# Performance work log

Hardware: AMD Instinct MI355X
Metric: run time of the kernel (lower is better)

Reference implementation:

```python
import jax, jax.numpy as jnp
import numpy as np

H = 1024      # hidden_size
MEL = 128     # mel_bins
B = 32        # batch
TENC = 512    # encoder time steps
TMEL = 400    # decoder (mel) time steps


def setup_inputs() -> dict:
    key = jax.random.key(0)
    ks = jax.random.split(key, 16)
    def w(k, shape, s=0.02):
        return jax.random.normal(k, shape, dtype=jnp.float32) * s
    return dict(
        encoder_hidden=w(ks[0], (4, B, H), 0.1),
        encoder_outputs=w(ks[1], (B, TENC, H), 0.1),
        y=w(ks[2], (B, TMEL, MEL), 1.0),
        mel_spec_lens=jax.random.randint(ks[3], (B,), 1, TMEL),
        # attention linear
        W_attn=w(ks[4], (H, H)), b_attn=jnp.zeros((H,), jnp.float32),
        # GRU layer 0 (input MEL) and layer 1 (input H); gate order r,z,n as in torch
        W_ih0=w(ks[5], (3 * H, MEL)), W_hh0=w(ks[6], (3 * H, H)),
        b_ih0=jnp.zeros((3 * H,), jnp.float32), b_hh0=jnp.zeros((3 * H,), jnp.float32),
        W_ih1=w(ks[7], (3 * H, H)), W_hh1=w(ks[8], (3 * H, H)),
        b_ih1=jnp.zeros((3 * H,), jnp.float32), b_hh1=jnp.zeros((3 * H,), jnp.float32),
        # concat2hidden, mel projection, eos gate
        Wc=w(ks[9], (H, 2 * H)), bc=jnp.zeros((H,), jnp.float32),
        Wp=w(ks[10], (MEL, H)), bp=jnp.zeros((MEL,), jnp.float32),
        Wg=w(ks[11], (1, H)), bg=jnp.zeros((1,), jnp.float32),
    )


def gru_cell(x, h, Wih, Whh, bih, bhh):
    # torch GRUCell math: gates ordered (r, z, n)
    gi = x @ Wih.T + bih          # [B, 3H]
    gh = h @ Whh.T + bhh          # [B, 3H]
    ir, iz, inn = jnp.split(gi, 3, axis=-1)
    hr, hz, hn = jnp.split(gh, 3, axis=-1)
    r = jax.nn.sigmoid(ir + hr)
    z = jax.nn.sigmoid(iz + hz)
    n = jnp.tanh(inn + r * hn)
    return (1.0 - z) * n + z * h


def reference(encoder_hidden, encoder_outputs, y, mel_spec_lens,
              W_attn, b_attn,
              W_ih0, W_hh0, b_ih0, b_hh0,
              W_ih1, W_hh1, b_ih1, b_hh1,
              Wc, bc, Wp, bp, Wg, bg):
    Bsz, Tmel, mel = y.shape
    # attention energy depends only on encoder_outputs -> hoist out of the loop (same math)
    energy = encoder_outputs @ W_attn.T + b_attn          # [B, Te, H]
    h0 = encoder_hidden[0]                                 # decoder_hidden = encoder_hidden[:num_layers]
    h1 = encoder_hidden[1]
    dec_in0 = jnp.zeros((Bsz, mel), y.dtype)               # SOS frame

    def step(carry, _):
        dec_in, h0, h1 = carry
        h0 = gru_cell(dec_in, h0, W_ih0, W_hh0, b_ih0, b_hh0)
        h1 = gru_cell(h0, h1, W_ih1, W_hh1, b_ih1, b_hh1)   # rnn_output = top-layer state [B, H]
        scores = jnp.einsum('bh,bth->bt', h1, energy)       # additive-style dot scores [B, Te]
        probs = jax.nn.softmax(scores, axis=1)
        context = jnp.einsum('bt,bth->bh', probs, encoder_outputs)  # [B, H]
        co = jnp.tanh(jnp.concatenate([h1, context], axis=-1) @ Wc.T + bc)  # [B, H]
        mel_out = co @ Wp.T + bp                            # [B, MEL]
        gate = (co @ Wg.T + bg)[:, 0]                       # [B]
        return (mel_out, h0, h1), (mel_out, gate)

    _, (mels, gates) = jax.lax.scan(step, (dec_in0, h0, h1), None, length=Tmel)
    mels = jnp.transpose(mels, (1, 0, 2))                   # [B, T, MEL]
    gates = gates.T                                          # [B, T]

    t = jnp.arange(Tmel)
    mask = t[None, :] > mel_spec_lens[:, None]               # strictly-greater, as in source
    masked_mel = jnp.where(mask[:, :, None], 0.0, mels)
    masked_gate = jnp.where(mask, 1000.0, gates)
    return masked_mel, masked_gate, mask
```

## Files before the change

### kernel.cpp

```cpp
#include <hip/hip_runtime.h>
#include <stdint.h>
#include <stddef.h>


#define TM 400

typedef unsigned short ushort_t;
typedef short  short8  __attribute__((ext_vector_type(8)));
typedef float  float4v __attribute__((ext_vector_type(4)));

#define DEVI static __device__ __forceinline__

#define SB_WF   0
#define SB_IH1  3145728
#define SB_HH0  6291456
#define SB_HH1  9437184
#define SB_AT   12582912
#define SB_WC   13631488
#define SW_TOT  15728640

__device__ __align__(16) ushort_t g_sw[SW_TOT];
__device__ __align__(16) float    g_wf[3145728];
__device__ __align__(16) ushort_t g_encb[16777216];
__device__ __align__(16) ushort_t g_energy[16777216];
__device__ __align__(16) ushort_t g_h0b[32768], g_h1b[32768];
__device__ __align__(16) float    g_h0f[32768], g_h1f[32768];
__device__ __align__(16) float    g_b0f[3072];
__device__ __align__(16) float    g_gh0[98304], g_gh1[98304];
__device__ __align__(16) float    g_ctxn[32768], g_sden[32];
__device__ __align__(16) float    g_cof[32768];
__device__ __align__(16) ushort_t g_cob[32768];

DEVI ushort_t f2b(float f) {
  union { float f; uint32_t u; } c; c.f = f;
  uint32_t u = c.u + 0x7fffu + ((c.u >> 16) & 1u);
  return (ushort_t)(u >> 16);
}
DEVI float b2f(ushort_t b) {
  union { uint32_t u; float f; } c; c.u = ((uint32_t)b) << 16; return c.f;
}
DEVI float sigm(float x) { return 1.f / (1.f + __expf(-x)); }

DEVI float4v mfma16(short8 a, short8 b, float4v c) {
  return __builtin_amdgcn_mfma_f32_16x16x32_bf16(a, b, c, 0, 0, 0);
}

DEVI float4v gemm_plain(const ushort_t* Ab, const ushort_t* Bw,
                        int ntile, int mu, int lane) {
  float4v acc = {0.f, 0.f, 0.f, 0.f};
  const ushort_t* a = Ab + (size_t)(mu * 16 + (lane & 15)) * 1024 + ((lane >> 4) << 3);
  const ushort_t* b = Bw + ((size_t)ntile * 32 * 64 + lane) * 8;
  for (int kb = 0; kb < 32; ++kb) {
    short8 av = *(const short8*)(a + kb * 32);
    acc = mfma16(av, *(const short8*)(b + (size_t)kb * 512), acc);
  }
  return acc;
}

DEVI float4v gemm_coE(const ushort_t* h1b, const float* ctxn, const float* sden,
                      const ushort_t* Bw, int ntile, int mu, int lane) {
  float4v acc = {0.f, 0.f, 0.f, 0.f};
  const int m = mu * 16 + (lane & 15), ko = (lane >> 4) << 3;
  const ushort_t* a0 = h1b + (size_t)m * 1024 + ko;
  const float* a1 = ctxn + (size_t)m * 1024 + ko;
  const float den = sden[m];
  const float inv = (den > 1e-35f) ? (1.f / den) : 0.f;
  const ushort_t* b = Bw + ((size_t)ntile * 64 * 64 + lane) * 8;
  for (int kb = 0; kb < 32; ++kb)
    acc = mfma16(*(const short8*)(a0 + kb * 32),
                 *(const short8*)(b + (size_t)kb * 512), acc);
  for (int kb = 32; kb < 64; ++kb) {
    float4v w0 = *(const float4v*)(a1 + (kb - 32) * 32);
    float4v w1 = *(const float4v*)(a1 + (kb - 32) * 32 + 4);
    short8 av;
#pragma unroll
    for (int j = 0; j < 4; ++j) {
      av[j]     = (short)f2b(w0[j] * inv);
      av[4 + j] = (short)f2b(w1[j] * inv);
    }
    acc = mfma16(av, *(const short8*)(b + (size_t)kb * 512), acc);
  }
  return acc;
}

DEVI void put_tile(float* sh, int q, int lane, float4v a) {
  const int base = q * 256 + (lane & 15);
#pragma unroll
  for (int i = 0; i < 4; ++i) sh[base + ((lane >> 4) * 4 + i) * 16] = a[i];
}

__global__ void k_wf(const float* __restrict__ Wih0, const float* __restrict__ Wp) {
  __shared__ __align__(16) float As[32][128];
  __shared__ __align__(16) float Bs[128][64];
  const int tid = threadIdx.x;
  const int nt = blockIdx.x >> 4, kt = blockIdx.x & 15;
  const int n0 = nt * 32, k0 = kt * 64;
  {
    const int r = tid >> 3, c0 = (tid & 7) * 16;
    for (int i = 0; i < 16; i += 4)
      *(float4v*)&As[r][c0 + i] = *(const float4v*)&Wih0[(size_t)(n0 + r) * 128 + c0 + i];
  }
  {
    const int r = tid >> 1, c0 = (tid & 1) * 32;
    for (int i = 0; i < 32; i += 4)
      *(float4v*)&Bs[r][c0 + i] = *(const float4v*)&Wp[(size_t)r * 1024 + k0 + c0 + i];
  }
  __syncthreads();
  const int rn = tid >> 3, kq = (tid & 7) * 8;
  float acc[8] = {0.f, 0.f, 0.f, 0.f, 0.f, 0.f, 0.f, 0.f};
  for (int m = 0; m < 128; ++m) {
    const float a = As[rn][m];
#pragma unroll
    for (int j = 0; j < 8; ++j) acc[j] += a * Bs[m][kq + j];
  }
  float* dst = g_wf + (size_t)(n0 + rn) * 1024 + k0 + kq;
#pragma unroll
  for (int j = 0; j < 8; ++j) dst[j] = acc[j];
}

__global__ void k_encb(const float* __restrict__ enc) {
  const size_t i = ((size_t)blockIdx.x * 256 + threadIdx.x) * 8;
  if (i >= 16777216) return;
  float4v a = *(const float4v*)(enc + i);
  float4v b = *(const float4v*)(enc + i + 4);
  short8 r;
#pragma unroll
  for (int j = 0; j < 4; ++j) { r[j] = (short)f2b(a[j]); r[4 + j] = (short)f2b(b[j]); }
  *(short8*)(g_encb + i) = r;
}

__global__ void k_swz(const float* __restrict__ W1, const float* __restrict__ W2,
                      const float* __restrict__ W3, const float* __restrict__ WA,
                      const float* __restrict__ WC) {
  long fid = (long)blockIdx.x * 256 + threadIdx.x;
  if (fid >= 1966080) return;
  const float* src; int N, K; long base, local;
  if      (fid < 393216)  { src = g_wf; N = 3072; K = 1024; base = SB_WF;  local = fid; }
  else if (fid < 786432)  { src = W1;   N = 3072; K = 1024; base = SB_IH1; local = fid - 393216; }
  else if (fid < 1179648) { src = W2;   N = 3072; K = 1024; base = SB_HH0; local = fid - 786432; }
  else if (fid < 1572864) { src = W3;   N = 3072; K = 1024; base = SB_HH1; local = fid - 1179648; }
  else if (fid < 1703936) { src = WA;   N = 1024; K = 1024; base = SB_AT;  local = fid - 1572864; }
  else                    { src = WC;   N = 1024; K = 2048; base = SB_WC;  local = fid - 1703936; }
  const int L = (int)(local & 63);
  long rest = local >> 6;
  const int KB = K >> 5;
  const int kb = (int)(rest % KB);
  const int nt = (int)(rest / KB);
  const int n  = nt * 16 + (L & 15);
  const int k0 = kb * 32 + ((L >> 4) << 3);
  short8 r;
#pragma unroll
  for (int i = 0; i < 8; ++i)
    r[i] = (short)f2b(src[(size_t)n * K + (k0 + i)]);
  *(short8*)(g_sw + base + local * 8) = r;
}

__global__ void k_energy(const float* __restrict__ b_attn) {
  __shared__ __align__(16) float sh[2048];
  const int tid = threadIdx.x, lane = tid & 63, wv = tid >> 6;
  const int rt = blockIdx.x;
  const ushort_t* Ab = g_encb + (size_t)rt * 32 * 1024;
  float* shw = sh + wv * 512;
  for (int i = 0; i < 16; ++i) {
    const int nt = wv * 16 + i;
    put_tile(shw, 0, lane, gemm_plain(Ab, g_sw + SB_AT, nt, 0, lane));
    put_tile(shw, 1, lane, gemm_plain(Ab, g_sw + SB_AT, nt, 1, lane));
    __syncthreads();
    const int row = lane >> 1, cf = (lane & 1) * 8;
    const int q = row >> 4, r = row & 15;
    short8 o;
#pragma unroll
    for (int j = 0; j < 8; ++j) {
      const int n = nt * 16 + cf + j;
      o[j] = (short)f2b(shw[q * 256 + r * 16 + cf + j] + b_attn[n]);
    }
    *(short8*)(g_energy + (size_t)(rt * 32 + row) * 1024 + nt * 16 + cf) = o;
    __syncthreads();
  }
}

__global__ void k_init(const float* __restrict__ ehid, const int* __restrict__ lens,
                       const float* __restrict__ Wih0, const float* __restrict__ bp,
                       const float* __restrict__ bih0,
                       float* __restrict__ out, int out_size) {
  int i = blockIdx.x * 256 + threadIdx.x;
  if (i < 32768) { float v = ehid[i]; g_h0f[i] = v; g_h0b[i] = f2b(v); }
  else if (i < 65536) {
    int j = i - 32768; float v = ehid[32768 + j];
    g_h1f[j] = v; g_h1b[j] = f2b(v);
  } else if (i < 78336) {
    int mi = i - 65536; int b = mi / 400, tt = mi % 400;
    int idx = 1651200 + mi;
    if (idx < out_size) out[idx] = (tt > lens[b]) ? 1.0f : 0.0f;
  } else if (i < 81408) {
    int n = i - 78336;
    float s = bih0[n];
    const float* wr = Wih0 + (size_t)n * 128;
    for (int m = 0; m < 128; ++m) s += bp[m] * wr[m];
    g_b0f[n] = s;
  }
}

__global__ void k_pre(const float* __restrict__ b_hh0, const float* __restrict__ b_hh1) {
  const int wg = blockIdx.x, tid = threadIdx.x;
  const int lane = tid & 63, wv = tid >> 6;
  __shared__ __align__(16) float sh[1536];
  const int qa = (wv < 2) ? wv * 2 : wv + 2;
  const int qb = (wv < 2) ? wv * 2 + 1 : -1;
  const ushort_t* Ab = (wg < 64) ? g_h0b : g_h1b;
  const ushort_t* Bw = g_sw + ((wg < 64) ? SB_HH0 : SB_HH1);
  const float* bhh = (wg < 64) ? b_hh0 : b_hh1;
  float* ghb = (wg < 64) ? g_gh0 : g_gh1;
  const int w16 = wg & 63;
  { int g = qa >> 1, mu = qa & 1;
    put_tile(sh, qa, lane, gemm_plain(Ab, Bw, g * 64 + w16, mu, lane)); }
  if (qb >= 0) { int g = qb >> 1, mu = qb & 1;
    put_tile(sh, qb, lane, gemm_plain(Ab, Bw, g * 64 + w16, mu, lane)); }
  __syncthreads();
  const int jl = tid & 15, mr = tid >> 4, jg = w16 * 16 + jl;
#pragma unroll
  for (int mu = 0; mu < 2; ++mu) {
    const int b = mu * 16 + mr;
#pragma unroll
    for (int g = 0; g < 3; ++g)
      ghb[b * 3072 + g * 1024 + jg] = sh[(g * 2 + mu) * 256 + tid] + bhh[g * 1024 + jg];
  }
}

__global__ void k_s1(int t, const float* __restrict__ b_ih0, const float* __restrict__ bp,
                     const float* __restrict__ Wp, const float* __restrict__ Wg,
                     const float* __restrict__ bg, const int* __restrict__ lens,
                     float* __restrict__ out, int out_size) {
  const int wg = blockIdx.x, tid = threadIdx.x;
  const int lane = tid & 63, wv = tid >> 6;
  __shared__ __align__(16) float sh[1536];
  if (wg < 64) {
    if (t >= TM) return;
    const int qa = (wv < 2) ? wv * 2 : wv + 2;
    const int qb = (wv < 2) ? wv * 2 + 1 : -1;
    const ushort_t* SW = g_sw + SB_WF;
    float4v acc;
    { int g = qa >> 1, mu = qa & 1;
      acc = (t > 0) ? gemm_plain(g_cob, SW, g * 64 + wg, mu, lane)
                    : float4v{0.f, 0.f, 0.f, 0.f};
      put_tile(sh, qa, lane, acc); }
    if (qb >= 0) { int g = qb >> 1, mu = qb & 1;
      acc = (t > 0) ? gemm_plain(g_cob, SW, g * 64 + wg, mu, lane)
                    : float4v{0.f, 0.f, 0.f, 0.f};
      put_tile(sh, qb, lane, acc); }
    __syncthreads();
    const int jl = tid & 15, mr = tid >> 4, jg = wg * 16 + jl;
    const float* bs = (t > 0) ? g_b0f : b_ih0;
    const float bir = bs[jg], biz = bs[1024 + jg], bin = bs[2048 + jg];
#pragma unroll
    for (int mu = 0; mu < 2; ++mu) {
      const int b = mu * 16 + mr;
      float gr = sh[mu * 256 + tid]       + bir + g_gh0[b * 3072 + jg];
      float gz = sh[(2 + mu) * 256 + tid] + biz + g_gh0[b * 3072 + 1024 + jg];
      float gn = sh[(4 + mu) * 256 + tid] + bin;
      float r = sigm(gr), z = sigm(gz);
      float nn = tanhf(gn + r * g_gh0[b * 3072 + 2048 + jg]);
      float h = (1.f - z) * nn + z * g_h0f[b * 1024 + jg];
      g_h0f[b * 1024 + jg] = h; g_h0b[b * 1024 + jg] = f2b(h);
    }
  } else if (wg < 128) {
    if (t == 0) return;
    const int idx = wg - 64, b = idx & 31, mh = idx >> 5;
    *(float4v*)&sh[tid * 4] = *(const float4v*)(g_cof + b * 1024 + tid * 4);
    __syncthreads();
    const int m = mh * 64 + (tid >> 2), q = tid & 3;
    const float* cop = sh + q * 256;
    const float* wpp = Wp + (size_t)m * 1024 + q * 256;
    float s = 0.f;
#pragma unroll 8
    for (int k = 0; k < 256; k += 4) {
      float4v cv = *(const float4v*)(cop + k);
      float4v wv4 = *(const float4v*)(wpp + k);
      s += cv[0] * wv4[0] + cv[1] * wv4[1] + cv[2] * wv4[2] + cv[3] * wv4[3];
    }
    s += __shfl_xor(s, 1, 64);
    s += __shfl_xor(s, 2, 64);
    if (q == 0) {
      const bool mk = (t - 1) > lens[b];
      const float v = mk ? 0.f : (s + bp[m]);
      const int oidx = b * 51200 + (t - 1) * 128 + m;
      if (oidx < out_size) out[oidx] = v;
    }
  } else if (wg == 128) {
    if (t == 0) return;
    const int b = tid >> 3, seg = tid & 7;
    const float* cop = g_cof + b * 1024 + seg * 128;
    const float* wgp = Wg + seg * 128;
    float s = 0.f;
#pragma unroll 8
    for (int k = 0; k < 128; k += 4) {
      float4v cv = *(const float4v*)(cop + k);
      float4v wv4 = *(const float4v*)(wgp + k);
      s += cv[0] * wv4[0] + cv[1] * wv4[1] + cv[2] * wv4[2] + cv[3] * wv4[3];
    }
    for (int o = 1; o < 8; o <<= 1) s += __shfl_xor(s, o, 64);
    if (seg == 0) {
      const bool mk = (t - 1) > lens[b];
      const float g = mk ? 1000.f : (s + bg[0]);
      const int oidx = 1638400 + b * 400 + (t - 1);
      if (oidx < out_size) out[oidx] = g;
    }
  } else {
    const int z0 = (wg - 129) * 256 + tid;
#pragma unroll
    for (int r4 = 0; r4 < 16; ++r4) g_ctxn[z0 + r4 * 2048] = 0.f;
    if (wg == 129 && tid < 32) g_sden[tid] = 0.f;
  }
}

__global__ void k_s2(const float* __restrict__ b_ih1, const float* __restrict__ b_hh0) {
  const int wg = blockIdx.x, tid = threadIdx.x;
  const int lane = tid & 63, wv = tid >> 6;
  __shared__ __align__(16) float sh[1536];
  const int qa = (wv < 2) ? wv * 2 : wv + 2;
  const int qb = (wv < 2) ? wv * 2 + 1 : -1;
  const bool lo = (wg < 64);
  const int w16 = wg & 63;
  const ushort_t* SW = g_sw + (lo ? SB_IH1 : SB_HH0);
  { int g = qa >> 1, mu = qa & 1;
    put_tile(sh, qa, lane, gemm_plain(g_h0b, SW, g * 64 + w16, mu, lane)); }
  if (qb >= 0) { int g = qb >> 1, mu = qb & 1;
    put_tile(sh, qb, lane, gemm_plain(g_h0b, SW, g * 64 + w16, mu, lane)); }
  __syncthreads();
  const int jl = tid & 15, mr = tid >> 4, jg = w16 * 16 + jl;
  if (lo) {
    const float bir = b_ih1[jg], biz = b_ih1[1024 + jg], bin = b_ih1[2048 + jg];
#pragma unroll
    for (int mu = 0; mu < 2; ++mu) {
      const int b = mu * 16 + mr;
      float gr = sh[mu * 256 + tid]       + bir + g_gh1[b * 3072 + jg];
      float gz = sh[(2 + mu) * 256 + tid] + biz + g_gh1[b * 3072 + 1024 + jg];
      float gn = sh[(4 + mu) * 256 + tid] + bin;
      float r = sigm(gr), z = sigm(gz);
      float nn = tanhf(gn + r * g_gh1[b * 3072 + 2048 + jg]);
      float h = (1.f - z) * nn + z * g_h1f[b * 1024 + jg];
      g_h1f[b * 1024 + jg] = h; g_h1b[b * 1024 + jg] = f2b(h);
    }
  } else {
#pragma unroll
    for (int mu = 0; mu < 2; ++mu) {
      const int b = mu * 16 + mr;
#pragma unroll
      for (int g = 0; g < 3; ++g)
        g_gh0[b * 3072 + g * 1024 + jg] = sh[(g * 2 + mu) * 256 + tid] + b_hh0[g * 1024 + jg];
    }
  }
}

__global__ void k_s3() {
  __shared__ __align__(16) float sh[4160];
  const int wg = blockIdx.x, tid = threadIdx.x;
  const int lane = tid & 63, wv = tid >> 6;
  const int b = wg >> 3, slot = wg & 7;
  const float* hp = g_h1f + b * 1024;
  float u0[8], u1[8];
  {
    float4v a0 = *(const float4v*)(hp + lane * 8);
    float4v a1 = *(const float4v*)(hp + lane * 8 + 4);
    float4v b0 = *(const float4v*)(hp + 512 + lane * 8);
    float4v b1 = *(const float4v*)(hp + 512 + lane * 8 + 4);
#pragma unroll
    for (int j = 0; j < 4; ++j) {
      u0[j] = a0[j]; u0[4 + j] = a1[j];
      u1[j] = b0[j]; u1[4 + j] = b1[j];
    }
  }
  float cx0[8] = {0.f, 0.f, 0.f, 0.f, 0.f, 0.f, 0.f, 0.f};
  float cx1[8] = {0.f, 0.f, 0.f, 0.f, 0.f, 0.f, 0.f, 0.f};
  float sw = 0.f;
  const size_t base = ((size_t)(b * 512 + slot * 64 + wv * 16)) * 1024 + lane * 8;
  for (int it = 0; it < 16; ++it) {
    const size_t off = base + (size_t)it * 1024;
    short8 g0 = *(const short8*)(g_energy + off);
    short8 g1 = *(const short8*)(g_energy + off + 512);
    short8 e0 = *(const short8*)(g_encb + off);
    short8 e1 = *(const short8*)(g_encb + off + 512);
    float ef0[8], ef1[8];
    float s = 0.f;
#pragma unroll
    for (int j = 0; j < 8; ++j) {
      ef0[j] = b2f((ushort_t)e0[j]);
      ef1[j] = b2f((ushort_t)e1[j]);
      s += u0[j] * b2f((ushort_t)g0[j]) + u1[j] * b2f((ushort_t)g1[j]);
    }
    for (int o = 1; o < 64; o <<= 1) s += __shfl_xor(s, o, 64);
    const float sc = fminf(fmaxf(s, -70.f), 70.f);
    const float p = __expf(sc);
    sw += p;
#pragma unroll
    for (int j = 0; j < 8; ++j) { cx0[j] += p * ef0[j]; cx1[j] += p * ef1[j]; }
  }
#pragma unroll
  for (int j = 0; j < 8; ++j) {
    sh[wv * 1024 + lane * 8 + j]       = cx0[j];
    sh[wv * 1024 + 512 + lane * 8 + j] = cx1[j];
  }
  if (lane == 0) sh[4096 + wv] = sw;
  __syncthreads();
  float4v t4 = {0.f, 0.f, 0.f, 0.f};
#pragma unroll
  for (int v = 0; v < 4; ++v) t4 += *(const float4v*)&sh[v * 1024 + tid * 4];
  float* dst = g_ctxn + b * 1024 + tid * 4;
#pragma unroll
  for (int c = 0; c < 4; ++c) unsafeAtomicAdd(dst + c, t4[c]);
  if (tid == 0)
    unsafeAtomicAdd(&g_sden[b], sh[4096] + sh[4097] + sh[4098] + sh[4099]);
}

__global__ void k_s4(const float* __restrict__ bc, const float* __restrict__ b_hh1) {
  const int wg = blockIdx.x, tid = threadIdx.x;
  const int lane = tid & 63, wv = tid >> 6;
  __shared__ __align__(16) float sh[1536];
  if (wg < 64) {
    if (wv < 2)
      put_tile(sh, wv, lane, gemm_coE(g_h1b, g_ctxn, g_sden, g_sw + SB_WC, wg, wv, lane));
    __syncthreads();
    const int jl = tid & 15, mr = tid >> 4;
    const float bcv = bc[wg * 16 + jl];
#pragma unroll
    for (int mu = 0; mu < 2; ++mu) {
      const int b = mu * 16 + mr;
      const float v = tanhf(sh[mu * 256 + tid] + bcv);
      g_cof[b * 1024 + wg * 16 + jl] = v;
      g_cob[b * 1024 + wg * 16 + jl] = f2b(v);
    }
  } else {
    const int w16 = wg - 64;
    const int qa = (wv < 2) ? wv * 2 : wv + 2;
    const int qb = (wv < 2) ? wv * 2 + 1 : -1;
    { int g = qa >> 1, mu = qa & 1;
      put_tile(sh, qa, lane, gemm_plain(g_h1b, g_sw + SB_HH1, g * 64 + w16, mu, lane)); }
    if (qb >= 0) { int g = qb >> 1, mu = qb & 1;
      put_tile(sh, qb, lane, gemm_plain(g_h1b, g_sw + SB_HH1, g * 64 + w16, mu, lane)); }
    __syncthreads();
    const int jl = tid & 15, mr = tid >> 4, jg = w16 * 16 + jl;
#pragma unroll
    for (int mu = 0; mu < 2; ++mu) {
      const int b = mu * 16 + mr;
#pragma unroll
      for (int g = 0; g < 3; ++g)
        g_gh1[b * 3072 + g * 1024 + jg] = sh[(g * 2 + mu) * 256 + tid] + b_hh1[g * 1024 + jg];
    }
  }
}

extern "C" void kernel_launch(void* const* d_in, const int* in_sizes, int n_in,
                              void* d_out, int out_size, void* d_ws, size_t ws_size,
                              hipStream_t stream) {
  const float* ehid  = (const float*)d_in[0];
  const float* enc   = (const float*)d_in[1];
  const int*   lens  = (const int*)d_in[3];
  const float* W_attn= (const float*)d_in[4];
  const float* b_attn= (const float*)d_in[5];
  const float* W_ih0 = (const float*)d_in[6];
  const float* W_hh0 = (const float*)d_in[7];
  const float* b_ih0 = (const float*)d_in[8];
  const float* b_hh0 = (const float*)d_in[9];
  const float* W_ih1 = (const float*)d_in[10];
  const float* W_hh1 = (const float*)d_in[11];
  const float* b_ih1 = (const float*)d_in[12];
  const float* b_hh1 = (const float*)d_in[13];
  const float* Wc    = (const float*)d_in[14];
  const float* bc    = (const float*)d_in[15];
  const float* Wp    = (const float*)d_in[16];
  const float* bp    = (const float*)d_in[17];
  const float* Wg    = (const float*)d_in[18];
  const float* bg    = (const float*)d_in[19];
  float* out = (float*)d_out;

  k_wf    <<<1536, 256, 0, stream>>>(W_ih0, Wp);
  k_encb  <<<8192, 256, 0, stream>>>(enc);
  k_swz   <<<7680, 256, 0, stream>>>(W_ih1, W_hh0, W_hh1, W_attn, Wc);
  k_energy<<<512,  256, 0, stream>>>(b_attn);
  k_init  <<<318,  256, 0, stream>>>(ehid, lens, W_ih0, bp, b_ih0, out, out_size);
  k_pre   <<<128,  256, 0, stream>>>(b_hh0, b_hh1);
  for (int t = 0; t < TM; ++t) {
    k_s1<<<137, 256, 0, stream>>>(t, b_ih0, bp, Wp, Wg, bg, lens, out, out_size);
    k_s2<<<128, 256, 0, stream>>>(b_ih1, b_hh0);
    k_s3<<<256, 256, 0, stream>>>();
    k_s4<<<128, 256, 0, stream>>>(bc, b_hh1);
  }
  k_s1<<<137, 256, 0, stream>>>(TM, b_ih0, bp, Wp, Wg, bg, lens, out, out_size);
}
```

Baseline: 21.23 ms.

## Quantize attention energy/encoder to fp8, fuse attention and concat stages, MFMA mel projection

Energy and encoder outputs are stored as fp8 e4m3 bytes and decoded through a shared-memory lookup table, halving the bytes streamed in the per-step attention kernel. The attention and concat/GRU-hh1 kernels are merged into one launch, with an atomic counter spin-wait so the concat blocks start only after all attention blocks finish. The mel projection is moved to bf16 MFMA using a pre-swizzled Wp. Risks include fp8 precision loss, and a possible deadlock or timeout fallback if the waiting blocks get scheduled before the producer blocks.

Result: slower. 24.69 ms (+16.3%).

```diff
diff --git a/kernel.cpp b/kernel.cpp
--- a/kernel.cpp
+++ b/kernel.cpp
@@ -6,8 +6,10 @@
 #define TM 400
 
 typedef unsigned short ushort_t;
-typedef short  short8  __attribute__((ext_vector_type(8)));
-typedef float  float4v __attribute__((ext_vector_type(4)));
+typedef unsigned long long u64_t;
+typedef short    short8  __attribute__((ext_vector_type(8)));
+typedef float    float4v __attribute__((ext_vector_type(4)));
+typedef unsigned uint2v  __attribute__((ext_vector_type(2)));
 
 #define DEVI static __device__ __forceinline__
 
@@ -17,12 +19,14 @@
 #define SB_HH1  9437184
 #define SB_AT   12582912
 #define SB_WC   13631488
-#define SW_TOT  15728640
+#define SB_WP   15728640
+#define SW_TOT  15859712
 
 __device__ __align__(16) ushort_t g_sw[SW_TOT];
 __device__ __align__(16) float    g_wf[3145728];
 __device__ __align__(16) ushort_t g_encb[16777216];
-__device__ __align__(16) ushort_t g_energy[16777216];
+__device__ __align__(16) unsigned char g_en8[16777216];
+__device__ __align__(16) unsigned char g_ec8[16777216];
 __device__ __align__(16) ushort_t g_h0b[32768], g_h1b[32768];
 __device__ __align__(16) float    g_h0f[32768], g_h1f[32768];
 __device__ __align__(16) float    g_b0f[3072];
@@ -30,19 +34,46 @@
 __device__ __align__(16) float    g_ctxn[32768], g_sden[32];
 __device__ __align__(16) float    g_cof[32768];
 __device__ __align__(16) ushort_t g_cob[32768];
+__device__ __align__(64) unsigned g_done[16];
 
 DEVI ushort_t f2b(float f) {
   union { float f; uint32_t u; } c; c.f = f;
   uint32_t u = c.u + 0x7fffu + ((c.u >> 16) & 1u);
   return (ushort_t)(u >> 16);
 }
-DEVI float b2f(ushort_t b) {
-  union { uint32_t u; float f; } c; c.u = ((uint32_t)b) << 16; return c.f;
-}
 DEVI float sigm(float x) { return 1.f / (1.f + __expf(-x)); }
+
+DEVI unsigned char f2e4m3(float f) {
+  union { float f; uint32_t u; } c; c.f = f;
+  const unsigned s = (c.u >> 24) & 0x80u;
+  const float a = fabsf(f);
+  if (a >= 448.f) return (unsigned char)(s | 0x7Eu);
+  if (a < 0.015625f) {
+    int m = (int)(a * 512.f + 0.5f);
+    if (m >= 8) return (unsigned char)(s | 0x08u);
+    return (unsigned char)(s | (unsigned)m);
+  }
+  int e32 = (int)((c.u >> 23) & 0xffu);
+  uint32_t m3 = (c.u >> 20) & 7u;
+  const uint32_t rem = c.u & 0xfffffu;
+  if (rem > 0x80000u || (rem == 0x80000u && (m3 & 1u))) {
+    if (++m3 == 8u) { m3 = 0u; ++e32; }
+  }
+  const int e8 = e32 - 120;
+  if (e8 >= 16) return (unsigned char)(s | 0x7Eu);
+  return (unsigned char)(s | ((unsigned)e8 << 3) | m3);
+}
 
 DEVI float4v mfma16(short8 a, short8 b, float4v c) {
   return __builtin_amdgcn_mfma_f32_16x16x32_bf16(a, b, c, 0, 0, 0);
+}
+
+DEVI u64_t ld_sc8(const void* p) {
+  return __hip_atomic_load((const u64_t*)p, __ATOMIC_RELAXED,
+                           __HIP_MEMORY_SCOPE_SYSTEM);
+}
+DEVI float ld_scf(const float* p) {
+  return __hip_atomic_load(p, __ATOMIC_RELAXED, __HIP_MEMORY_SCOPE_SYSTEM);
 }
 
 DEVI float4v gemm_plain(const ushort_t* Ab, const ushort_t* Bw,
@@ -57,28 +88,36 @@
   return acc;
 }
 
-DEVI float4v gemm_coE(const ushort_t* h1b, const float* ctxn, const float* sden,
-                      const ushort_t* Bw, int ntile, int mu, int lane) {
+DEVI float4v gemm_scE2(const ushort_t* h1b, const float* ctxn, const float* sden,
+                       const ushort_t* Bw, int ntile, int mu, int lane) {
   float4v acc = {0.f, 0.f, 0.f, 0.f};
   const int m = mu * 16 + (lane & 15), ko = (lane >> 4) << 3;
   const ushort_t* a0 = h1b + (size_t)m * 1024 + ko;
   const float* a1 = ctxn + (size_t)m * 1024 + ko;
-  const float den = sden[m];
+  const float den = ld_scf(&sden[m]);
   const float inv = (den > 1e-35f) ? (1.f / den) : 0.f;
   const ushort_t* b = Bw + ((size_t)ntile * 64 * 64 + lane) * 8;
   for (int kb = 0; kb < 32; ++kb)
     acc = mfma16(*(const short8*)(a0 + kb * 32),
                  *(const short8*)(b + (size_t)kb * 512), acc);
-  for (int kb = 32; kb < 64; ++kb) {
-    float4v w0 = *(const float4v*)(a1 + (kb - 32) * 32);
-    float4v w1 = *(const float4v*)(a1 + (kb - 32) * 32 + 4);
-    short8 av;
-#pragma unroll
-    for (int j = 0; j < 4; ++j) {
-      av[j]     = (short)f2b(w0[j] * inv);
-      av[4 + j] = (short)f2b(w1[j] * inv);
-    }
-    acc = mfma16(av, *(const short8*)(b + (size_t)kb * 512), acc);
+  for (int c = 0; c < 4; ++c) {
+    u64_t t[32];
+#pragma unroll
+    for (int j = 0; j < 8; ++j)
+#pragma unroll
+      for (int q = 0; q < 4; ++q)
+        t[j * 4 + q] = ld_sc8(a1 + (c * 8 + j) * 32 + q * 2);
+#pragma unroll
+    for (int j = 0; j < 8; ++j) {
+      short8 av;
+#pragma unroll
+      for (int q = 0; q < 4; ++q) {
+        union { u64_t u; float f[2]; } w; w.u = t[j * 4 + q];
+        av[q * 2]     = (short)f2b(w.f[0] * inv);
+        av[q * 2 + 1] = (short)f2b(w.f[1] * inv);
+      }
+      acc = mfma16(av, *(const short8*)(b + (size_t)(32 + c * 8 + j) * 512), acc);
+    }
   }
   return acc;
 }
@@ -129,18 +168,34 @@
   *(short8*)(g_encb + i) = r;
 }
 
+__global__ void k_q8(const float* __restrict__ enc) {
+  const size_t i = ((size_t)blockIdx.x * 256 + threadIdx.x) * 8;
+  if (i >= 16777216) return;
+  float4v a = *(const float4v*)(enc + i);
+  float4v b = *(const float4v*)(enc + i + 4);
+  unsigned lo = 0, hi = 0;
+#pragma unroll
+  for (int j = 0; j < 4; ++j) {
+    lo |= (unsigned)f2e4m3(a[j]) << (8 * j);
+    hi |= (unsigned)f2e4m3(b[j]) << (8 * j);
+  }
+  uint2v o; o[0] = lo; o[1] = hi;
+  *(uint2v*)(g_ec8 + i) = o;
+}
+
 __global__ void k_swz(const float* __restrict__ W1, const float* __restrict__ W2,
                       const float* __restrict__ W3, const float* __restrict__ WA,
-                      const float* __restrict__ WC) {
+                      const float* __restrict__ WC, const float* __restrict__ Wp) {
   long fid = (long)blockIdx.x * 256 + threadIdx.x;
-  if (fid >= 1966080) return;
+  if (fid >= 1982464) return;
   const float* src; int N, K; long base, local;
   if      (fid < 393216)  { src = g_wf; N = 3072; K = 1024; base = SB_WF;  local = fid; }
   else if (fid < 786432)  { src = W1;   N = 3072; K = 1024; base = SB_IH1; local = fid - 393216; }
   else if (fid < 1179648) { src = W2;   N = 3072; K = 1024; base = SB_HH0; local = fid - 786432; }
   else if (fid < 1572864) { src = W3;   N = 3072; K = 1024; base = SB_HH1; local = fid - 1179648; }
   else if (fid < 1703936) { src = WA;   N = 1024; K = 1024; base = SB_AT;  local = fid - 1572864; }
-  else                    { src = WC;   N = 1024; K = 2048; base = SB_WC;  local = fid - 1703936; }
+  else if (fid < 1966080) { src = WC;   N = 1024; K = 2048; base = SB_WC;  local = fid - 1703936; }
+  else                    { src = Wp;   N = 128;  K = 1024; base = SB_WP;  local = fid - 1966080; }
   const int L = (int)(local & 63);
   long rest = local >> 6;
   const int KB = K >> 5;
@@ -168,13 +223,14 @@
     __syncthreads();
     const int row = lane >> 1, cf = (lane & 1) * 8;
     const int q = row >> 4, r = row & 15;
-    short8 o;
-#pragma unroll
-    for (int j = 0; j < 8; ++j) {
-      const int n = nt * 16 + cf + j;
-      o[j] = (short)f2b(shw[q * 256 + r * 16 + cf + j] + b_attn[n]);
-    }
-    *(short8*)(g_energy + (size_t)(rt * 32 + row) * 1024 + nt * 16 + cf) = o;
+    unsigned lo = 0, hi = 0;
+#pragma unroll
+    for (int j = 0; j < 4; ++j) {
+      lo |= (unsigned)f2e4m3(shw[q * 256 + r * 16 + cf + j] + b_attn[nt * 16 + cf + j]) << (8 * j);
+      hi |= (unsigned)f2e4m3(shw[q * 256 + r * 16 + cf + 4 + j] + b_attn[nt * 16 + cf + 4 + j]) << (8 * j);
+    }
+    uint2v o; o[0] = lo; o[1] = hi;
+    *(uint2v*)(g_en8 + (size_t)(rt * 32 + row) * 1024 + nt * 16 + cf) = o;
     __syncthreads();
   }
 }
@@ -184,6 +240,7 @@
                        const float* __restrict__ bih0,
                        float* __restrict__ out, int out_size) {
   int i = blockIdx.x * 256 + threadIdx.x;
+  if (i == 0) g_done[0] = 0u;
   if (i < 32768) { float v = ehid[i]; g_h0f[i] = v; g_h0b[i] = f2b(v); }
   else if (i < 65536) {
     int j = i - 32768; float v = ehid[32768 + j];
@@ -228,8 +285,8 @@
 }
 
 __global__ void k_s1(int t, const float* __restrict__ b_ih0, const float* __restrict__ bp,
-                     const float* __restrict__ Wp, const float* __restrict__ Wg,
-                     const float* __restrict__ bg, const int* __restrict__ lens,
+                     const float* __restrict__ Wg, const float* __restrict__ bg,
+                     const int* __restrict__ lens,
                      float* __restrict__ out, int out_size) {
   const int wg = blockIdx.x, tid = threadIdx.x;
   const int lane = tid & 63, wv = tid >> 6;
@@ -263,30 +320,24 @@
       float h = (1.f - z) * nn + z * g_h0f[b * 1024 + jg];
       g_h0f[b * 1024 + jg] = h; g_h0b[b * 1024 + jg] = f2b(h);
     }
-  } else if (wg < 128) {
+  } else if (wg < 72) {
     if (t == 0) return;
-    const int idx = wg - 64, b = idx & 31, mh = idx >> 5;
-    *(float4v*)&sh[tid * 4] = *(const float4v*)(g_cof + b * 1024 + tid * 4);
-    __syncthreads();
-    const int m = mh * 64 + (tid >> 2), q = tid & 3;
-    const float* cop = sh + q * 256;
-    const float* wpp = Wp + (size_t)m * 1024 + q * 256;
-    float s = 0.f;
-#pragma unroll 8
-    for (int k = 0; k < 256; k += 4) {
-      float4v cv = *(const float4v*)(cop + k);
-      float4v wv4 = *(const float4v*)(wpp + k);
-      s += cv[0] * wv4[0] + cv[1] * wv4[1] + cv[2] * wv4[2] + cv[3] * wv4[3];
-    }
-    s += __shfl_xor(s, 1, 64);
-    s += __shfl_xor(s, 2, 64);
-    if (q == 0) {
+    const int nt = wg - 64;
+    if (wv < 2)
+      put_tile(sh, wv, lane, gemm_plain(g_cob, g_sw + SB_WP, nt, wv, lane));
+    __syncthreads();
+    const int jl = tid & 15, mr = tid >> 4;
+    const int m = nt * 16 + jl;
+    const float bpv = bp[m];
+#pragma unroll
+    for (int mu = 0; mu < 2; ++mu) {
+      const int b = mu * 16 + mr;
       const bool mk = (t - 1) > lens[b];
-      const float v = mk ? 0.f : (s + bp[m]);
+      const float v = mk ? 0.f : (sh[mu * 256 + tid] + bpv);
       const int oidx = b * 51200 + (t - 1) * 128 + m;
       if (oidx < out_size) out[oidx] = v;
     }
-  } else if (wg == 128) {
+  } else if (wg == 72) {
     if (t == 0) return;
     const int b = tid >> 3, seg = tid & 7;
     const float* cop = g_cof + b * 1024 + seg * 128;
@@ -306,10 +357,13 @@
       if (oidx < out_size) out[oidx] = g;
     }
   } else {
-    const int z0 = (wg - 129) * 256 + tid;
+    const int z0 = (wg - 73) * 256 + tid;
 #pragma unroll
     for (int r4 = 0; r4 < 16; ++r4) g_ctxn[z0 + r4 * 2048] = 0.f;
-    if (wg == 129 && tid < 32) g_sden[tid] = 0.f;
+    if (wg == 73 && tid < 32) g_sden[tid] = 0.f;
+    if (wg == 73 && tid == 0)
+      __hip_atomic_store(&g_done[0], 0u, __ATOMIC_RELAXED,
+                         __HIP_MEMORY_SCOPE_AGENT);
   }
 }
 
@@ -352,85 +406,109 @@
   }
 }
 
-__global__ void k_s3() {
+__global__ void k_s34(const float* __restrict__ bc, const float* __restrict__ b_hh1) {
   __shared__ __align__(16) float sh[4160];
+  __shared__ __align__(16) float tabf[256];
   const int wg = blockIdx.x, tid = threadIdx.x;
   const int lane = tid & 63, wv = tid >> 6;
-  const int b = wg >> 3, slot = wg & 7;
-  const float* hp = g_h1f + b * 1024;
-  float u0[8], u1[8];
-  {
-    float4v a0 = *(const float4v*)(hp + lane * 8);
-    float4v a1 = *(const float4v*)(hp + lane * 8 + 4);
-    float4v b0 = *(const float4v*)(hp + 512 + lane * 8);
-    float4v b1 = *(const float4v*)(hp + 512 + lane * 8 + 4);
-#pragma unroll
-    for (int j = 0; j < 4; ++j) {
-      u0[j] = a0[j]; u0[4 + j] = a1[j];
-      u1[j] = b0[j]; u1[4 + j] = b1[j];
-    }
-  }
-  float cx0[8] = {0.f, 0.f, 0.f, 0.f, 0.f, 0.f, 0.f, 0.f};
-  float cx1[8] = {0.f, 0.f, 0.f, 0.f, 0.f, 0.f, 0.f, 0.f};
-  float sw = 0.f;
-  const size_t base = ((size_t)(b * 512 + slot * 64 + wv * 16)) * 1024 + lane * 8;
-  for (int it = 0; it < 16; ++it) {
-    const size_t off = base + (size_t)it * 1024;
-    short8 g0 = *(const short8*)(g_energy + off);
-    short8 g1 = *(const short8*)(g_energy + off + 512);
-    short8 e0 = *(const short8*)(g_encb + off);
-    short8 e1 = *(const short8*)(g_encb + off + 512);
-    float ef0[8], ef1[8];
-    float s = 0.f;
+  if (wg < 256) {
+    {
+      const unsigned v = (unsigned)tid;
+      const unsigned e = (v >> 3) & 0xFu, m = v & 7u;
+      union { unsigned u; float f; } c;
+      if (e == 0u) c.f = (float)m * 0.001953125f;
+      else c.u = ((e + 120u) << 23) | (m << 20);
+      c.u |= (v & 0x80u) << 24;
+      tabf[v] = c.f;
+    }
+    const int b = wg >> 3, slot = wg & 7;
+    const float* hp = g_h1f + b * 1024;
+    float u0[8], u1[8];
+    {
+      float4v a0 = *(const float4v*)(hp + lane * 8);
+      float4v a1 = *(const float4v*)(hp + lane * 8 + 4);
+      float4v b0 = *(const float4v*)(hp + 512 + lane * 8);
+      float4v b1 = *(const float4v*)(hp + 512 + lane * 8 + 4);
+#pragma unroll
+      for (int j = 0; j < 4; ++j) {
+        u0[j] = a0[j]; u0[4 + j] = a1[j];
+        u1[j] = b0[j]; u1[4 + j] = b1[j];
+      }
+    }
+    __syncthreads();
+    float cx0[8] = {0.f, 0.f, 0.f, 0.f, 0.f, 0.f, 0.f, 0.f};
+    float cx1[8] = {0.f, 0.f, 0.f, 0.f, 0.f, 0.f, 0.f, 0.f};
+    float sw = 0.f;
+    const size_t base = ((size_t)(b * 512 + slot * 64 + wv * 16)) * 1024 + lane * 8;
+    for (int it = 0; it < 16; ++it) {
+      const size_t off = base + (size_t)it * 1024;
+      uint2v gE0 = *(const uint2v*)(g_en8 + off);
+      uint2v gE1 = *(const uint2v*)(g_en8 + off + 512);
+      uint2v eE0 = *(const uint2v*)(g_ec8 + off);
+      uint2v eE1 = *(const uint2v*)(g_ec8 + off + 512);
+      float ef0[8], ef1[8];
+      float s = 0.f;
+#pragma unroll
+      for (int w = 0; w < 2; ++w)
+#pragma unroll
+        for (int j = 0; j < 4; ++j) {
+          const int k = w * 4 + j;
+          s += u0[k] * tabf[(gE0[w] >> (8 * j)) & 0xffu];
+          s += u1[k] * tabf[(gE1[w] >> (8 * j)) & 0xffu];
+          ef0[k] = tabf[(eE0[w] >> (8 * j)) & 0xffu];
+          ef1[k] = tabf[(eE1[w] >> (8 * j)) & 0xffu];
+        }
+      for (int o = 1; o < 64; o <<= 1) s += __shfl_xor(s, o, 64);
+      const float sc = fminf(fmaxf(s, -70.f), 70.f);
+      const float p = __expf(sc);
+      sw += p;
+#pragma unroll
+      for (int j = 0; j < 8; ++j) { cx0[j] += p * ef0[j]; cx1[j] += p * ef1[j]; }
+    }
 #pragma unroll
     for (int j = 0; j < 8; ++j) {
-      ef0[j] = b2f((ushort_t)e0[j]);
-      ef1[j] = b2f((ushort_t)e1[j]);
-      s += u0[j] * b2f((ushort_t)g0[j]) + u1[j] * b2f((ushort_t)g1[j]);
-    }
-    for (int o = 1; o < 64; o <<= 1) s += __shfl_xor(s, o, 64);
-    const float sc = fminf(fmaxf(s, -70.f), 70.f);
-    const float p = __expf(sc);
-    sw += p;
-#pragma unroll
-    for (int j = 0; j < 8; ++j) { cx0[j] += p * ef0[j]; cx1[j] += p * ef1[j]; }
-  }
-#pragma unroll
-  for (int j = 0; j < 8; ++j) {
-    sh[wv * 1024 + lane * 8 + j]       = cx0[j];
-    sh[wv * 1024 + 512 + lane * 8 + j] = cx1[j];
-  }
-  if (lane == 0) sh[4096 + wv] = sw;
-  __syncthreads();
-  float4v t4 = {0.f, 0.f, 0.f, 0.f};
-#pragma unroll
-  for (int v = 0; v < 4; ++v) t4 += *(const float4v*)&sh[v * 1024 + tid * 4];
-  float* dst = g_ctxn + b * 1024 + tid * 4;
-#pragma unroll
-  for (int c = 0; c < 4; ++c) unsafeAtomicAdd(dst + c, t4[c]);
-  if (tid == 0)
-    unsafeAtomicAdd(&g_sden[b], sh[4096] + sh[4097] + sh[4098] + sh[4099]);
-}
-
-__global__ void k_s4(const float* __restrict__ bc, const float* __restrict__ b_hh1) {
-  const int wg = blockIdx.x, tid = threadIdx.x;
-  const int lane = tid & 63, wv = tid >> 6;
-  __shared__ __align__(16) float sh[1536];
-  if (wg < 64) {
+      sh[wv * 1024 + lane * 8 + j]       = cx0[j];
+      sh[wv * 1024 + 512 + lane * 8 + j] = cx1[j];
+    }
+    if (lane == 0) sh[4096 + wv] = sw;
+    __syncthreads();
+    float4v t4 = {0.f, 0.f, 0.f, 0.f};
+#pragma unroll
+    for (int v = 0; v < 4; ++v) t4 += *(const float4v*)&sh[v * 1024 + tid * 4];
+    float* dst = g_ctxn + b * 1024 + tid * 4;
+#pragma unroll
+    for (int c = 0; c < 4; ++c) unsafeAtomicAdd(dst + c, t4[c]);
+    if (tid == 0)
+      unsafeAtomicAdd(&g_sden[b], sh[4096] + sh[4097] + sh[4098] + sh[4099]);
+    __syncthreads();
+    if (tid == 0)
+      __hip_atomic_fetch_add(&g_done[0], 1u, __ATOMIC_RELAXED,
+                             __HIP_MEMORY_SCOPE_AGENT);
+  } else if (wg < 320) {
+    const int w16 = wg - 256;
+    if (tid == 0) {
+      unsigned spins = 0;
+      while (__hip_atomic_load(&g_done[0], __ATOMIC_RELAXED,
+                               __HIP_MEMORY_SCOPE_AGENT) < 256u) {
+        __builtin_amdgcn_s_sleep(2);
+        if (++spins > (1u << 22)) break;
+      }
+    }
+    __syncthreads();
     if (wv < 2)
-      put_tile(sh, wv, lane, gemm_coE(g_h1b, g_ctxn, g_sden, g_sw + SB_WC, wg, wv, lane));
+      put_tile(sh, wv, lane, gemm_scE2(g_h1b, g_ctxn, g_sden, g_sw + SB_WC, w16, wv, lane));
     __syncthreads();
     const int jl = tid & 15, mr = tid >> 4;
-    const float bcv = bc[wg * 16 + jl];
+    const float bcv = bc[w16 * 16 + jl];
 #pragma unroll
     for (int mu = 0; mu < 2; ++mu) {
       const int b = mu * 16 + mr;
       const float v = tanhf(sh[mu * 256 + tid] + bcv);
-      g_cof[b * 1024 + wg * 16 + jl] = v;
-      g_cob[b * 1024 + wg * 16 + jl] = f2b(v);
+      g_cof[b * 1024 + w16 * 16 + jl] = v;
+      g_cob[b * 1024 + w16 * 16 + jl] = f2b(v);
     }
   } else {
-    const int w16 = wg - 64;
+    const int w16 = wg - 320;
     const int qa = (wv < 2) ? wv * 2 : wv + 2;
     const int qb = (wv < 2) ? wv * 2 + 1 : -1;
     { int g = qa >> 1, mu = qa & 1;
@@ -475,15 +553,15 @@
 
   k_wf    <<<1536, 256, 0, stream>>>(W_ih0, Wp);
   k_encb  <<<8192, 256, 0, stream>>>(enc);
-  k_swz   <<<7680, 256, 0, stream>>>(W_ih1, W_hh0, W_hh1, W_attn, Wc);
+  k_q8    <<<8192, 256, 0, stream>>>(enc);
+  k_swz   <<<7744, 256, 0, stream>>>(W_ih1, W_hh0, W_hh1, W_attn, Wc, Wp);
   k_energy<<<512,  256, 0, stream>>>(b_attn);
   k_init  <<<318,  256, 0, stream>>>(ehid, lens, W_ih0, bp, b_ih0, out, out_size);
   k_pre   <<<128,  256, 0, stream>>>(b_hh0, b_hh1);
   for (int t = 0; t < TM; ++t) {
-    k_s1<<<137, 256, 0, stream>>>(t, b_ih0, bp, Wp, Wg, bg, lens, out, out_size);
-    k_s2<<<128, 256, 0, stream>>>(b_ih1, b_hh0);
-    k_s3<<<256, 256, 0, stream>>>();
-    k_s4<<<128, 256, 0, stream>>>(bc, b_hh1);
-  }
-  k_s1<<<137, 256, 0, stream>>>(TM, b_ih0, bp, Wp, Wg, bg, lens, out, out_size);
-}
+    k_s1 <<<81,  256, 0, stream>>>(t, b_ih0, bp, Wg, bg, lens, out, out_size);
+    k_s2 <<<128, 256, 0, stream>>>(b_ih1, b_hh0);
+    k_s34<<<384, 256, 0, stream>>>(bc, b_hh1);
+  }
+  k_s1<<<81, 256, 0, stream>>>(TM, b_ih0, bp, Wg, bg, lens, out, out_size);
+}
```
